# Performance work log

Measured on AMD Instinct MI355X. Metric: run time of the kernel, lower is better.

The kernel has to match this reference:

```python
import jax, jax.numpy as jnp
import numpy as np

B = 2048   # batch
C = 64     # EEG channels (num_eegch)
T = 125    # time samples -> pool5 -> 25 -> (p=5, 5)
H = 8      # num_heads
L = 6      # num_layers
D = 16     # num_projected_features
QK = 8     # qkv_len
P = 5      # tokens before cls
EPS = 1e-5


def setup_inputs() -> dict:
    key = jax.random.key(0)
    ks = iter(jax.random.split(key, 64))

    def nrm(shape, s=0.05):
        return jax.random.normal(next(ks), shape, jnp.float32) * s

    return {
        "x": jax.random.normal(next(ks), (B, 1, C, T), jnp.float32),
        "conv_t_w": nrm((8, 1, 1, 63)),
        "conv_t_b": nrm((8,)),
        "bn1_g": 1.0 + nrm((8,)),
        "bn1_b": nrm((8,)),
        "bn1_m": nrm((8,)),
        "bn1_v": 1.0 + 0.1 * jax.random.uniform(next(ks), (8,), jnp.float32),
        "conv_s_w": nrm((16, 1, C, 1)),
        "conv_s_b": nrm((16,)),
        "bn2_g": 1.0 + nrm((16,)),
        "bn2_b": nrm((16,)),
        "bn2_m": nrm((16,)),
        "bn2_v": 1.0 + 0.1 * jax.random.uniform(next(ks), (16,), jnp.float32),
        "proj_w": nrm((D, 16 * 5)),
        "proj_b": nrm((D,)),
        "cls_token": nrm((1, 1, D), 1.0),
        "pe": nrm((1, P + 1, D), 1.0),
        "qkv_w": nrm((L, 3 * H * QK, D)),
        "qkv_b": nrm((L, 3 * H * QK)),
        "out_w": nrm((L, D, H * QK)),
        "out_b": nrm((L, D)),
        "ln1_g": jnp.ones((L, D), jnp.float32),
        "ln1_b": jnp.zeros((L, D), jnp.float32),
        "ln2_g": jnp.ones((L, D), jnp.float32),
        "ln2_b": jnp.zeros((L, D), jnp.float32),
        "mlp_w1": nrm((L, 2 * D, D)),
        "mlp_b1": nrm((L, 2 * D)),
        "mlp_w2": nrm((L, D, 2 * D)),
        "mlp_b2": nrm((L, D)),
        "head_ln_g": jnp.ones((D,), jnp.float32),
        "head_ln_b": jnp.zeros((D,), jnp.float32),
        "head_w": nrm((2, D)),
        "head_b": nrm((2,)),
    }


def _bn(z, g, b, m, v):
    s = (g * jax.lax.rsqrt(v + EPS))[None, :, None, None]
    return (z - m[None, :, None, None]) * s + b[None, :, None, None]


def _ln(z, g, b):
    m = z.mean(-1, keepdims=True)
    var = jnp.mean((z - m) ** 2, -1, keepdims=True)
    return (z - m) * jax.lax.rsqrt(var + EPS) * g + b


def _forward(x, conv_t_w, conv_t_b, bn1_g, bn1_b, bn1_m, bn1_v,
             conv_s_w, conv_s_b, bn2_g, bn2_b, bn2_m, bn2_v,
             proj_w, proj_b, cls_token, pe,
             qkv_w, qkv_b, out_w, out_b, ln1_g, ln1_b, ln2_g, ln2_b,
             mlp_w1, mlp_b1, mlp_w2, mlp_b2,
             head_ln_g, head_ln_b, head_w, head_b):
    b = x.shape[0]
    dn = ('NCHW', 'OIHW', 'NCHW')
    # temporal conv, 'same' padding on width (kernel 63 -> pad 31/31)
    y = jax.lax.conv_general_dilated(x, conv_t_w, (1, 1), [(0, 0), (31, 31)], dimension_numbers=dn)
    y = _bn(y + conv_t_b[None, :, None, None], bn1_g, bn1_b, bn1_m, bn1_v)
    # grouped spatial conv collapses the EEG-channel axis
    y = jax.lax.conv_general_dilated(y, conv_s_w, (1, 1), 'VALID', dimension_numbers=dn, feature_group_count=8)
    y = _bn(y + conv_s_b[None, :, None, None], bn2_g, bn2_b, bn2_m, bn2_v)
    y = jax.nn.elu(y)                              # (b,16,1,125)
    y = y.reshape(b, 16, 1, T // 5, 5).mean(-1)    # avg_pool2d (1,5) -> (b,16,1,25)
    # dropout: identity at inference
    y = y.reshape(b, 16, 1, P, 5)
    y = jnp.swapaxes(y, 3, 4)
    tok = jnp.swapaxes(y.reshape(b, 16 * 5, P), 1, 2)   # (b,5,80)
    tok = tok @ proj_w.T + proj_b                       # (b,5,16)
    z = jnp.concatenate([jnp.broadcast_to(cls_token, (b, 1, D)), tok], axis=1) + pe  # (b,6,16)
    scale = QK ** -0.5
    for i in range(L):
        h1 = _ln(z, ln1_g[i], ln1_b[i])
        qkv = h1 @ qkv_w[i].T + qkv_b[i]                # (b,6,3*H*QK)
        q, k, v = jnp.split(qkv, 3, axis=-1)
        q = q.reshape(b, P + 1, H, QK).transpose(0, 2, 1, 3)
        k = k.reshape(b, P + 1, H, QK).transpose(0, 2, 1, 3)
        v = v.reshape(b, P + 1, H, QK).transpose(0, 2, 1, 3)
        att = jax.nn.softmax(jnp.einsum('bhsd,bhtd->bhst', q, k) * scale, axis=-1)
        o = jnp.einsum('bhst,bhtd->bhsd', att, v).transpose(0, 2, 1, 3).reshape(b, P + 1, H * QK)
        z = o @ out_w[i].T + out_b[i] + z
        h2 = _ln(z, ln2_g[i], ln2_b[i])
        m = jax.nn.gelu(h2 @ mlp_w1[i].T + mlp_b1[i], approximate=False) @ mlp_w2[i].T + mlp_b2[i]
        z = m + z
    cls = _ln(z[:, 0, :], head_ln_g, head_ln_b)
    return jax.nn.softmax(cls @ head_w.T + head_b, axis=-1)


def reference(x, conv_t_w, conv_t_b, bn1_g, bn1_b, bn1_m, bn1_v,
              conv_s_w, conv_s_b, bn2_g, bn2_b, bn2_m, bn2_v,
              proj_w, proj_b, cls_token, pe,
              qkv_w, qkv_b, out_w, out_b, ln1_g, ln1_b, ln2_g, ln2_b,
              mlp_w1, mlp_b1, mlp_w2, mlp_b2,
              head_ln_g, head_ln_b, head_w, head_b):
    return _forward(x, conv_t_w, conv_t_b, bn1_g, bn1_b, bn1_m, bn1_v,
                    conv_s_w, conv_s_b, bn2_g, bn2_b, bn2_m, bn2_v,
                    proj_w, proj_b, cls_token, pe,
                    qkv_w, qkv_b, out_w, out_b, ln1_g, ln1_b, ln2_g, ln2_b,
                    mlp_w1, mlp_b1, mlp_w2, mlp_b2,
                    head_ln_g, head_ln_b, head_w, head_b)
```

## Files before the change

### kernel.cpp

```cpp
#include <hip/hip_runtime.h>

#define WAVE_SYNC() do { asm volatile("" ::: "memory"); \
                         __builtin_amdgcn_wave_barrier(); \
                         asm volatile("" ::: "memory"); } while (0)

typedef _Float16 h2 __attribute__((ext_vector_type(2)));
typedef _Float16 h4 __attribute__((ext_vector_type(4)));
typedef _Float16 h8 __attribute__((ext_vector_type(8)));

__device__ __forceinline__ float fdot2(h2 a, h2 b, float c) {
#if defined(__has_builtin)
#if __has_builtin(__builtin_amdgcn_fdot2)
    return __builtin_amdgcn_fdot2(a, b, c, false);
#else
    return (float)a[0]*(float)b[0] + (float)a[1]*(float)b[1] + c;
#endif
#else
    return (float)a[0]*(float)b[0] + (float)a[1]*(float)b[1] + c;
#endif
}

__device__ __forceinline__ float dot8h(h8 a, h8 b, float c) {
    float s = c;
    #pragma unroll
    for (int i = 0; i < 4; ++i) {
        h2 x = {a[2*i], a[2*i+1]};
        h2 y = {b[2*i], b[2*i+1]};
        s = fdot2(x, y, s);
    }
    return s;
}

__device__ __forceinline__ float dot16h(h8 a0, h8 a1, h8 b0, h8 b1, float c) {
    return dot8h(a1, b1, dot8h(a0, b0, c));
}

__device__ __forceinline__ float ln_norm16(float z, float g, float bb) {
    float s = z, q = z * z;
    #pragma unroll
    for (int off = 8; off >= 1; off >>= 1) {
        s += __shfl_xor(s, off, 16);
        q += __shfl_xor(q, off, 16);
    }
    float mean = s * 0.0625f;
    float var  = q * 0.0625f - mean * mean;
    return (z - mean) * rsqrtf(var + 1e-5f) * g + bb;
}

__device__ __forceinline__ float gelu_exact(float a) {
    float xa = fabsf(a) * 0.70710678118654752f;
    float tt = 1.f / (1.f + 0.3275911f * xa);
    float poly = tt * (0.254829592f + tt * (-0.284496736f + tt * (1.421413741f
               + tt * (-1.453152027f + tt * 1.061405429f))));
    float erfv = 1.f - poly * __expf(-xa * xa);
    erfv = a >= 0.f ? erfv : -erfv;
    return 0.5f * a * (1.f + erfv);
}

#define F5_XSTR 210
#define F5_PF   1680
#define F5_WLH  8000
#define F5_TOTF 4512

extern "C" __global__ __launch_bounds__(128, 2)
void eegnet_frontend(
    const float* __restrict__ x,
    const float* __restrict__ conv_t_w, const float* __restrict__ conv_t_b,
    const float* __restrict__ bn1_g, const float* __restrict__ bn1_b,
    const float* __restrict__ bn1_m, const float* __restrict__ bn1_v,
    const float* __restrict__ conv_s_w, const float* __restrict__ conv_s_b,
    const float* __restrict__ bn2_g, const float* __restrict__ bn2_b,
    const float* __restrict__ bn2_m, const float* __restrict__ bn2_v,
    const float* __restrict__ proj_w, const float* __restrict__ proj_b,
    float* __restrict__ tokws)
{
    __shared__ __align__(16) float sm[F5_TOTF];
    _Float16* smh = reinterpret_cast<_Float16*>(sm);
    const int b   = blockIdx.x;
    const int tid = threadIdx.x;

    {
        const float4* xb4 = reinterpret_cast<const float4*>(x + (size_t)b * 8000);
        #pragma unroll
        for (int k = 0; k < 16; ++k) {
            int g = min(tid + k * 128, 1999);
            float4 v = xb4[g];
            h4 hv = {(_Float16)v.x, (_Float16)v.y, (_Float16)v.z, (_Float16)v.w};
            *reinterpret_cast<h4*>(&smh[4 * g]) = hv;
        }
    }
    {
        #pragma unroll
        for (int k = 0; k < 4; ++k) {
            int i  = tid + k * 128;
            int c2 = i & 31, o = i >> 5;
            float2 wv = *reinterpret_cast<const float2*>(conv_s_w + o * 64 + 2 * c2);
            h2 hp = {(_Float16)wv.x, (_Float16)wv.y};
            *reinterpret_cast<h2*>(&smh[F5_WLH + (c2 * 16 + o) * 2]) = hp;
        }
    }
    __syncthreads();

    float acc[16];
    #pragma unroll
    for (int o = 0; o < 16; ++o) acc[o] = 0.f;
    if (tid < 125) {
        #pragma unroll 4
        for (int c2 = 0; c2 < 32; ++c2) {
            h2 xp = { smh[(2 * c2) * 125 + tid], smh[(2 * c2 + 1) * 125 + tid] };
            const h8* wrow = reinterpret_cast<const h8*>(&smh[F5_WLH + c2 * 32]);
            h8 w0 = wrow[0], w1 = wrow[1], w2 = wrow[2], w3 = wrow[3];
            #pragma unroll
            for (int o = 0; o < 4; ++o) {
                h2 p0 = {w0[2*o], w0[2*o+1]};
                h2 p1 = {w1[2*o], w1[2*o+1]};
                h2 p2 = {w2[2*o], w2[2*o+1]};
                h2 p3 = {w3[2*o], w3[2*o+1]};
                acc[o]      = fdot2(p0, xp, acc[o]);
                acc[4 + o]  = fdot2(p1, xp, acc[4 + o]);
                acc[8 + o]  = fdot2(p2, xp, acc[8 + o]);
                acc[12 + o] = fdot2(p3, xp, acc[12 + o]);
            }
        }
    }
    __syncthreads();

    for (int i = tid; i < 16 * 85; i += 128) {
        int row = i / 85, k = i - row * 85;
        int off = (k < 32) ? k : (k + 125);
        smh[row * F5_XSTR + off] = (_Float16)0.f;
    }
    if (tid < 125) {
        #pragma unroll
        for (int o = 0; o < 16; ++o)
            smh[o * F5_XSTR + 32 + tid] = (_Float16)acc[o];
    }
    __syncthreads();

    const int oo = tid & 15, qg = tid >> 4, gg = oo >> 1;
    float sa, cc;
    {
        float s1 = bn1_g[gg] * rsqrtf(bn1_v[gg] + 1e-5f);
        float b1 = (conv_t_b[gg] - bn1_m[gg]) * s1 + bn1_b[gg];
        float s2 = bn2_g[oo] * rsqrtf(bn2_v[oo] + 1e-5f);
        float ssum = 0.f;
        const float4* csw = reinterpret_cast<const float4*>(conv_s_w + oo * 64);
        #pragma unroll
        for (int i = 0; i < 16; ++i) {
            float4 v = csw[i];
            ssum += v.x + v.y + v.z + v.w;
        }
        sa = s1 * s2;
        cc = (b1 * ssum + conv_s_b[oo] - bn2_m[oo]) * s2 + bn2_b[oo];
    }
    float wt[63];
    #pragma unroll
    for (int k = 0; k < 63; ++k) wt[k] = conv_t_w[gg * 63 + k];

    #pragma unroll 2
    for (int jj = 0; jj < 4; ++jj) {
        int j  = qg * 4 + jj;
        int jc = min(j, 24);
        int base = oo * F5_XSTR + 5 * jc + 1;
        float acc5[5] = {0.f, 0.f, 0.f, 0.f, 0.f};
        #pragma unroll
        for (int m = 0; m < 67; ++m) {
            float xv = (float)smh[base + m];
            #pragma unroll
            for (int u = 0; u < 5; ++u)
                if (u <= m && m - u <= 62) acc5[u] += wt[m - u] * xv;
        }
        float psum = 0.f;
        #pragma unroll
        for (int u = 0; u < 5; ++u) {
            float v = acc5[u] * sa + cc;
            psum += (v > 0.f) ? v : (__expf(v) - 1.f);
        }
        if (j == jc) sm[F5_PF + oo * 28 + j] = psum * 0.2f;
    }

    __syncthreads();

    if (tid < 80) {
        int p = tid >> 4, dd = tid & 15;
        float acc3 = proj_b[dd];
        const float4* wp = reinterpret_cast<const float4*>(proj_w + dd * 80);
        #pragma unroll
        for (int i = 0; i < 20; ++i) {
            float4 w4 = wp[i];
            acc3 += w4.x * sm[F5_PF + ((4*i+0)/5) * 28 + p * 5 + ((4*i+0)%5)];
            acc3 += w4.y * sm[F5_PF + ((4*i+1)/5) * 28 + p * 5 + ((4*i+1)%5)];
            acc3 += w4.z * sm[F5_PF + ((4*i+2)/5) * 28 + p * 5 + ((4*i+2)%5)];
            acc3 += w4.w * sm[F5_PF + ((4*i+3)/5) * 28 + p * 5 + ((4*i+3)%5)];
        }
        tokws[b * 80 + p * 16 + dd] = acc3;
    }
}

#define WQKVH 0
#define WOUTH 4608
#define WM1H  5760
#define WM2H  6528
#define BQKVF 3584
#define BOUTF 3776
#define BM1F  3792
#define BM2F  3824
#define LN1GF 3840
#define LN1BF 3856
#define LN2GF 3872
#define LN2BF 3888
#define SCR0  7808
#define SSTRH 1584
#define SH1H  0
#define SQKVH 144
#define SMHSH 1344
#define T_BYTES 18784

extern "C" __global__ __launch_bounds__(128, 2)
void eegnet_transformer(
    const float* __restrict__ cls_token, const float* __restrict__ pe,
    const float* __restrict__ qkv_w, const float* __restrict__ qkv_b,
    const float* __restrict__ out_w, const float* __restrict__ out_b,
    const float* __restrict__ ln1_g, const float* __restrict__ ln1_b,
    const float* __restrict__ ln2_g, const float* __restrict__ ln2_b,
    const float* __restrict__ mlp_w1, const float* __restrict__ mlp_b1,
    const float* __restrict__ mlp_w2, const float* __restrict__ mlp_b2,
    const float* __restrict__ head_ln_g, const float* __restrict__ head_ln_b,
    const float* __restrict__ head_w, const float* __restrict__ head_b,
    const float* __restrict__ tokws, float* __restrict__ out)
{
    __shared__ __align__(16) unsigned char smb[T_BYTES];
    float*    smf = reinterpret_cast<float*>(smb);
    _Float16* smh = reinterpret_cast<_Float16*>(smb);

    const int tid = threadIdx.x;
    const int sA  = blockIdx.x;
    const int d16 = tid & 15, qg = tid >> 4;
    const int t6c = min(qg, 5);
    const int wav = tid >> 6, al = tid & 63;
    const int sb  = SCR0;

    float zA;
    {
        float peV = pe[t6c * 16 + d16];
        if (t6c == 0) zA = cls_token[d16] + peV;
        else          zA = tokws[sA * 80 + (t6c - 1) * 16 + d16] + peV;
    }

    #pragma unroll 1
    for (int li = 0; li < 6; ++li) {
        __syncthreads();

        {
            const float4* s1 = reinterpret_cast<const float4*>(qkv_w + li * 3072);
            #pragma unroll
            for (int it = 0; it < 6; ++it) {
                int i = tid + it * 128;
                float4 v = s1[i];
                int j = i >> 2, k = (i & 3) << 2;
                h4 hv = {(_Float16)v.x, (_Float16)v.y, (_Float16)v.z, (_Float16)v.w};
                *reinterpret_cast<h4*>(&smh[WQKVH + j * 24 + k]) = hv;
            }
            const float4* s2 = reinterpret_cast<const float4*>(out_w + li * 1024);
            #pragma unroll
            for (int it = 0; it < 2; ++it) {
                int i = tid + it * 128;
                float4 v = s2[i];
                int j = i >> 4, k = (i & 15) << 2;
                h4 hv = {(_Float16)v.x, (_Float16)v.y, (_Float16)v.z, (_Float16)v.w};
                *reinterpret_cast<h4*>(&smh[WOUTH + j * 72 + k]) = hv;
            }
            {
                float4 v = reinterpret_cast<const float4*>(mlp_w1 + li * 512)[tid];
                int j = tid >> 2, k = (tid & 3) << 2;
                h4 hv = {(_Float16)v.x, (_Float16)v.y, (_Float16)v.z, (_Float16)v.w};
                *reinterpret_cast<h4*>(&smh[WM1H + j * 24 + k]) = hv;
            }
            {
                float4 v = reinterpret_cast<const float4*>(mlp_w2 + li * 512)[tid];
                int j = tid >> 3, k = (tid & 7) << 2;
                h4 hv = {(_Float16)v.x, (_Float16)v.y, (_Float16)v.z, (_Float16)v.w};
                *reinterpret_cast<h4*>(&smh[WM2H + j * 40 + k]) = hv;
            }
            #pragma unroll
            for (int p = 0; p < 2; ++p) {
                int i = tid + p * 128;
                if (i < 192)       smf[BQKVF + i]       = qkv_b[li * 192 + i];
                else if (i < 208)  smf[BOUTF + i - 192] = out_b[li * 16 + i - 192];
                else if (i < 240)  smf[BM1F + i - 208]  = mlp_b1[li * 32 + i - 208];
                else               smf[BM2F + i - 240]  = mlp_b2[li * 16 + i - 240];
            }
            if (tid >= 64 && tid < 80)        smf[LN1GF + tid - 64]  = ln1_g[li * 16 + tid - 64];
            else if (tid >= 80 && tid < 96)   smf[LN1BF + tid - 80]  = ln1_b[li * 16 + tid - 80];
            else if (tid >= 96 && tid < 112)  smf[LN2GF + tid - 96]  = ln2_g[li * 16 + tid - 96];
            else if (tid >= 112 && tid < 128) smf[LN2BF + tid - 112] = ln2_b[li * 16 + tid - 112];
        }
        __syncthreads();

        {
            float g = smf[LN1GF + d16], bb = smf[LN1BF + d16];
            smh[sb + SH1H + t6c * 24 + d16] = (_Float16)ln_norm16(zA, g, bb);
        }
        WAVE_SYNC();

        h8 hA0 = *reinterpret_cast<const h8*>(&smh[sb + SH1H + t6c * 24]);
        h8 hA1 = *reinterpret_cast<const h8*>(&smh[sb + SH1H + t6c * 24 + 8]);

        #pragma unroll 2
        for (int r = 0; r < 12; ++r) {
            int j = d16 + 16 * r;
            h8 w0 = *reinterpret_cast<const h8*>(&smh[WQKVH + j * 24]);
            h8 w1 = *reinterpret_cast<const h8*>(&smh[WQKVH + j * 24 + 8]);
            float bb = smf[BQKVF + j];
            smh[sb + SQKVH + t6c * 200 + j] = (_Float16)dot16h(hA0, hA1, w0, w1, bb);
        }
        __syncthreads();

        {
            bool act = (wav == 0) ? (al < 32) : (al < 16);
            if (act) {
                int h  = al & 7;
                int qs = (wav == 0) ? (al >> 3) : 4 + (al >> 3);
                const int qoff = sb + SQKVH + qs * 200 + h * 8;
                h8 qA = *reinterpret_cast<const h8*>(&smh[qoff]);
                float scA[6];
                #pragma unroll
                for (int t = 0; t < 6; ++t) {
                    h8 kA = *reinterpret_cast<const h8*>(&smh[sb + SQKVH + t * 200 + 64 + h * 8]);
                    scA[t] = dot8h(qA, kA, 0.f) * 0.35355339059327373f;
                }
                float mxA = scA[0];
                #pragma unroll
                for (int t = 1; t < 6; ++t) mxA = fmaxf(mxA, scA[t]);
                float suA = 0.f;
                #pragma unroll
                for (int t = 0; t < 6; ++t) { scA[t] = __expf(scA[t] - mxA); suA += scA[t]; }
                float ivA = 1.f / suA;
                h2 oA[4];
                #pragma unroll
                for (int k2 = 0; k2 < 4; ++k2) oA[k2] = h2{0, 0};
                #pragma unroll
                for (int t = 0; t < 6; ++t) {
                    h8 vA = *reinterpret_cast<const h8*>(&smh[sb + SQKVH + t * 200 + 128 + h * 8]);
                    _Float16 aa = (_Float16)(scA[t] * ivA);
                    h2 av = {aa, aa};
                    #pragma unroll
                    for (int k2 = 0; k2 < 4; ++k2) {
                        h2 va = {vA[2*k2], vA[2*k2+1]};
                        oA[k2] += av * va;
                    }
                }
                h8 stA;
                #pragma unroll
                for (int k2 = 0; k2 < 4; ++k2) {
                    stA[2*k2] = oA[k2][0]; stA[2*k2+1] = oA[k2][1];
                }
                *reinterpret_cast<h8*>(&smh[qoff]) = stA;
            }
        }
        WAVE_SYNC();

        {
            float aA = smf[BOUTF + d16];
            #pragma unroll
            for (int i = 0; i < 8; ++i) {
                h8 w  = *reinterpret_cast<const h8*>(&smh[WOUTH + d16 * 72 + 8 * i]);
                h8 va = *reinterpret_cast<const h8*>(&smh[sb + SQKVH + t6c * 200 + 8 * i]);
                aA = dot8h(va, w, aA);
            }
            zA += aA;
        }

        {
            float g = smf[LN2GF + d16], bb = smf[LN2BF + d16];
            smh[sb + SH1H + t6c * 24 + d16] = (_Float16)ln_norm16(zA, g, bb);
        }
        WAVE_SYNC();
        hA0 = *reinterpret_cast<const h8*>(&smh[sb + SH1H + t6c * 24]);
        hA1 = *reinterpret_cast<const h8*>(&smh[sb + SH1H + t6c * 24 + 8]);

        #pragma unroll
        for (int r = 0; r < 2; ++r) {
            int uu = d16 + 16 * r;
            h8 w0 = *reinterpret_cast<const h8*>(&smh[WM1H + uu * 24]);
            h8 w1 = *reinterpret_cast<const h8*>(&smh[WM1H + uu * 24 + 8]);
            float bb = smf[BM1F + uu];
            float aA = dot16h(hA0, hA1, w0, w1, bb);
            smh[sb + SMHSH + t6c * 40 + uu] = (_Float16)gelu_exact(aA);
        }
        WAVE_SYNC();

        {
            float aA = smf[BM2F + d16];
            #pragma unroll
            for (int i = 0; i < 4; ++i) {
                h8 w  = *reinterpret_cast<const h8*>(&smh[WM2H + d16 * 40 + 8 * i]);
                h8 va = *reinterpret_cast<const h8*>(&smh[sb + SMHSH + t6c * 40 + 8 * i]);
                aA = dot8h(va, w, aA);
            }
            zA += aA;
        }
    }

    if (tid < 16) {
        float g = head_ln_g[d16], bb = head_ln_b[d16];
        float w0 = head_w[d16], w1 = head_w[16 + d16];
        float cvA = ln_norm16(zA, g, bb);
        float pA0 = cvA * w0, pA1 = cvA * w1;
        #pragma unroll
        for (int off = 8; off >= 1; off >>= 1) {
            pA0 += __shfl_xor(pA0, off, 16);
            pA1 += __shfl_xor(pA1, off, 16);
        }
        if (tid == 0) {
            float l0 = pA0 + head_b[0], l1 = pA1 + head_b[1];
            float mx = fmaxf(l0, l1);
            float e0 = __expf(l0 - mx), e1 = __expf(l1 - mx);
            float inv = 1.f / (e0 + e1);
            out[sA * 2 + 0] = e0 * inv;
            out[sA * 2 + 1] = e1 * inv;
        }
    }
}

extern "C" void kernel_launch(void* const* d_in, const int* in_sizes, int n_in,
                              void* d_out, int out_size, void* d_ws, size_t ws_size,
                              hipStream_t stream) {
    (void)n_in; (void)ws_size; (void)out_size;
    const float* a0  = (const float*)d_in[0];
    const float* a1  = (const float*)d_in[1];
    const float* a2  = (const float*)d_in[2];
    const float* a3  = (const float*)d_in[3];
    const float* a4  = (const float*)d_in[4];
    const float* a5  = (const float*)d_in[5];
    const float* a6  = (const float*)d_in[6];
    const float* a7  = (const float*)d_in[7];
    const float* a8  = (const float*)d_in[8];
    const float* a9  = (const float*)d_in[9];
    const float* a10 = (const float*)d_in[10];
    const float* a11 = (const float*)d_in[11];
    const float* a12 = (const float*)d_in[12];
    const float* a13 = (const float*)d_in[13];
    const float* a14 = (const float*)d_in[14];
    const float* a15 = (const float*)d_in[15];
    const float* a16 = (const float*)d_in[16];
    const float* a17 = (const float*)d_in[17];
    const float* a18 = (const float*)d_in[18];
    const float* a19 = (const float*)d_in[19];
    const float* a20 = (const float*)d_in[20];
    const float* a21 = (const float*)d_in[21];
    const float* a22 = (const float*)d_in[22];
    const float* a23 = (const float*)d_in[23];
    const float* a24 = (const float*)d_in[24];
    const float* a25 = (const float*)d_in[25];
    const float* a26 = (const float*)d_in[26];
    const float* a27 = (const float*)d_in[27];
    const float* a28 = (const float*)d_in[28];
    const float* a29 = (const float*)d_in[29];
    const float* a30 = (const float*)d_in[30];
    const float* a31 = (const float*)d_in[31];
    const float* a32 = (const float*)d_in[32];

    int Bn = in_sizes[0] / (64 * 125);
    float* tokws = (float*)d_ws;

    eegnet_frontend<<<Bn, 128, 0, stream>>>(
        a0, a1, a2, a3, a4, a5, a6, a7, a8, a9, a10, a11, a12, a13, a14, tokws);

    eegnet_transformer<<<Bn, 128, 0, stream>>>(
        a15, a16, a17, a18, a19, a20, a21, a22, a23, a24, a25, a26, a27, a28,
        a29, a30, a31, a32, tokws, (float*)d_out);
}
```

Baseline: 240.0 us.

## Fuse EEG frontend and transformer into a single kernel

Merges the convolutional frontend and the transformer encoder into one kernel per batch element. Tokens are kept in shared memory instead of going through a global workspace, and the second launch is removed. The spatial conv switches from packed fp16 dot2 on shared-memory weights to fp32 FMAs reading weights directly from global memory. The temporal conv staging buffer is stored as fp32, and the shared-memory layout is reorganised to fit both stages.

```diff
diff --git a/kernel.cpp b/kernel.cpp
--- a/kernel.cpp
+++ b/kernel.cpp
@@ -57,145 +57,11 @@
     return 0.5f * a * (1.f + erfv);
 }
 
-#define F5_XSTR 210
-#define F5_PF   1680
-#define F5_WLH  8000
-#define F5_TOTF 4512
-
-extern "C" __global__ __launch_bounds__(128, 2)
-void eegnet_frontend(
-    const float* __restrict__ x,
-    const float* __restrict__ conv_t_w, const float* __restrict__ conv_t_b,
-    const float* __restrict__ bn1_g, const float* __restrict__ bn1_b,
-    const float* __restrict__ bn1_m, const float* __restrict__ bn1_v,
-    const float* __restrict__ conv_s_w, const float* __restrict__ conv_s_b,
-    const float* __restrict__ bn2_g, const float* __restrict__ bn2_b,
-    const float* __restrict__ bn2_m, const float* __restrict__ bn2_v,
-    const float* __restrict__ proj_w, const float* __restrict__ proj_b,
-    float* __restrict__ tokws)
-{
-    __shared__ __align__(16) float sm[F5_TOTF];
-    _Float16* smh = reinterpret_cast<_Float16*>(sm);
-    const int b   = blockIdx.x;
-    const int tid = threadIdx.x;
-
-    {
-        const float4* xb4 = reinterpret_cast<const float4*>(x + (size_t)b * 8000);
-        #pragma unroll
-        for (int k = 0; k < 16; ++k) {
-            int g = min(tid + k * 128, 1999);
-            float4 v = xb4[g];
-            h4 hv = {(_Float16)v.x, (_Float16)v.y, (_Float16)v.z, (_Float16)v.w};
-            *reinterpret_cast<h4*>(&smh[4 * g]) = hv;
-        }
-    }
-    {
-        #pragma unroll
-        for (int k = 0; k < 4; ++k) {
-            int i  = tid + k * 128;
-            int c2 = i & 31, o = i >> 5;
-            float2 wv = *reinterpret_cast<const float2*>(conv_s_w + o * 64 + 2 * c2);
-            h2 hp = {(_Float16)wv.x, (_Float16)wv.y};
-            *reinterpret_cast<h2*>(&smh[F5_WLH + (c2 * 16 + o) * 2]) = hp;
-        }
-    }
-    __syncthreads();
-
-    float acc[16];
-    #pragma unroll
-    for (int o = 0; o < 16; ++o) acc[o] = 0.f;
-    if (tid < 125) {
-        #pragma unroll 4
-        for (int c2 = 0; c2 < 32; ++c2) {
-            h2 xp = { smh[(2 * c2) * 125 + tid], smh[(2 * c2 + 1) * 125 + tid] };
-            const h8* wrow = reinterpret_cast<const h8*>(&smh[F5_WLH + c2 * 32]);
-            h8 w0 = wrow[0], w1 = wrow[1], w2 = wrow[2], w3 = wrow[3];
-            #pragma unroll
-            for (int o = 0; o < 4; ++o) {
-                h2 p0 = {w0[2*o], w0[2*o+1]};
-                h2 p1 = {w1[2*o], w1[2*o+1]};
-                h2 p2 = {w2[2*o], w2[2*o+1]};
-                h2 p3 = {w3[2*o], w3[2*o+1]};
-                acc[o]      = fdot2(p0, xp, acc[o]);
-                acc[4 + o]  = fdot2(p1, xp, acc[4 + o]);
-                acc[8 + o]  = fdot2(p2, xp, acc[8 + o]);
-                acc[12 + o] = fdot2(p3, xp, acc[12 + o]);
-            }
-        }
-    }
-    __syncthreads();
-
-    for (int i = tid; i < 16 * 85; i += 128) {
-        int row = i / 85, k = i - row * 85;
-        int off = (k < 32) ? k : (k + 125);
-        smh[row * F5_XSTR + off] = (_Float16)0.f;
-    }
-    if (tid < 125) {
-        #pragma unroll
-        for (int o = 0; o < 16; ++o)
-            smh[o * F5_XSTR + 32 + tid] = (_Float16)acc[o];
-    }
-    __syncthreads();
-
-    const int oo = tid & 15, qg = tid >> 4, gg = oo >> 1;
-    float sa, cc;
-    {
-        float s1 = bn1_g[gg] * rsqrtf(bn1_v[gg] + 1e-5f);
-        float b1 = (conv_t_b[gg] - bn1_m[gg]) * s1 + bn1_b[gg];
-        float s2 = bn2_g[oo] * rsqrtf(bn2_v[oo] + 1e-5f);
-        float ssum = 0.f;
-        const float4* csw = reinterpret_cast<const float4*>(conv_s_w + oo * 64);
-        #pragma unroll
-        for (int i = 0; i < 16; ++i) {
-            float4 v = csw[i];
-            ssum += v.x + v.y + v.z + v.w;
-        }
-        sa = s1 * s2;
-        cc = (b1 * ssum + conv_s_b[oo] - bn2_m[oo]) * s2 + bn2_b[oo];
-    }
-    float wt[63];
-    #pragma unroll
-    for (int k = 0; k < 63; ++k) wt[k] = conv_t_w[gg * 63 + k];
-
-    #pragma unroll 2
-    for (int jj = 0; jj < 4; ++jj) {
-        int j  = qg * 4 + jj;
-        int jc = min(j, 24);
-        int base = oo * F5_XSTR + 5 * jc + 1;
-        float acc5[5] = {0.f, 0.f, 0.f, 0.f, 0.f};
-        #pragma unroll
-        for (int m = 0; m < 67; ++m) {
-            float xv = (float)smh[base + m];
-            #pragma unroll
-            for (int u = 0; u < 5; ++u)
-                if (u <= m && m - u <= 62) acc5[u] += wt[m - u] * xv;
-        }
-        float psum = 0.f;
-        #pragma unroll
-        for (int u = 0; u < 5; ++u) {
-            float v = acc5[u] * sa + cc;
-            psum += (v > 0.f) ? v : (__expf(v) - 1.f);
-        }
-        if (j == jc) sm[F5_PF + oo * 28 + j] = psum * 0.2f;
-    }
-
-    __syncthreads();
-
-    if (tid < 80) {
-        int p = tid >> 4, dd = tid & 15;
-        float acc3 = proj_b[dd];
-        const float4* wp = reinterpret_cast<const float4*>(proj_w + dd * 80);
-        #pragma unroll
-        for (int i = 0; i < 20; ++i) {
-            float4 w4 = wp[i];
-            acc3 += w4.x * sm[F5_PF + ((4*i+0)/5) * 28 + p * 5 + ((4*i+0)%5)];
-            acc3 += w4.y * sm[F5_PF + ((4*i+1)/5) * 28 + p * 5 + ((4*i+1)%5)];
-            acc3 += w4.z * sm[F5_PF + ((4*i+2)/5) * 28 + p * 5 + ((4*i+2)%5)];
-            acc3 += w4.w * sm[F5_PF + ((4*i+3)/5) * 28 + p * 5 + ((4*i+3)%5)];
-        }
-        tokws[b * 80 + p * 16 + dd] = acc3;
-    }
-}
+
+#define F_XSTR 204
+#define F_PL   4000
+#define TOKF   4704
+#define FUSED_TOTF 4784
 
 #define WQKVH 0
 #define WOUTH 4608
@@ -210,14 +76,20 @@
 #define LN2GF 3872
 #define LN2BF 3888
 #define SCR0  7808
-#define SSTRH 1584
 #define SH1H  0
 #define SQKVH 144
 #define SMHSH 1344
-#define T_BYTES 18784
 
 extern "C" __global__ __launch_bounds__(128, 2)
-void eegnet_transformer(
+void eegnet_fused(
+    const float* __restrict__ x,
+    const float* __restrict__ conv_t_w, const float* __restrict__ conv_t_b,
+    const float* __restrict__ bn1_g, const float* __restrict__ bn1_b,
+    const float* __restrict__ bn1_m, const float* __restrict__ bn1_v,
+    const float* __restrict__ conv_s_w, const float* __restrict__ conv_s_b,
+    const float* __restrict__ bn2_g, const float* __restrict__ bn2_b,
+    const float* __restrict__ bn2_m, const float* __restrict__ bn2_v,
+    const float* __restrict__ proj_w, const float* __restrict__ proj_b,
     const float* __restrict__ cls_token, const float* __restrict__ pe,
     const float* __restrict__ qkv_w, const float* __restrict__ qkv_b,
     const float* __restrict__ out_w, const float* __restrict__ out_b,
@@ -227,24 +99,126 @@
     const float* __restrict__ mlp_w2, const float* __restrict__ mlp_b2,
     const float* __restrict__ head_ln_g, const float* __restrict__ head_ln_b,
     const float* __restrict__ head_w, const float* __restrict__ head_b,
-    const float* __restrict__ tokws, float* __restrict__ out)
+    float* __restrict__ out)
 {
-    __shared__ __align__(16) unsigned char smb[T_BYTES];
-    float*    smf = reinterpret_cast<float*>(smb);
-    _Float16* smh = reinterpret_cast<_Float16*>(smb);
+    __shared__ __align__(16) float sm[FUSED_TOTF];
+    _Float16* smh = reinterpret_cast<_Float16*>(sm);
+    _Float16* xr  = reinterpret_cast<_Float16*>(sm);
 
     const int tid = threadIdx.x;
-    const int sA  = blockIdx.x;
+    const int b   = blockIdx.x;
+
+    {
+        const float4* xb4 = reinterpret_cast<const float4*>(x + (size_t)b * 8000);
+        #pragma unroll
+        for (int k = 0; k < 16; ++k) {
+            int g = min(tid + k * 128, 1999);
+            float4 v = xb4[g];
+            h4 hv = {(_Float16)v.x, (_Float16)v.y, (_Float16)v.z, (_Float16)v.w};
+            *reinterpret_cast<h4*>(&xr[4 * g]) = hv;
+        }
+    }
+    __syncthreads();
+
+    float acc[16];
+    #pragma unroll
+    for (int o = 0; o < 16; ++o) acc[o] = 0.f;
+    {
+        const int t = min(tid, 124);
+        #pragma unroll 8
+        for (int c = 0; c < 64; ++c) {
+            float xv = (float)xr[c * 125 + t];
+            #pragma unroll
+            for (int o = 0; o < 16; ++o)
+                acc[o] += conv_s_w[o * 64 + c] * xv;
+        }
+    }
+    __syncthreads();
+
+    for (int i = tid; i < 16 * 79; i += 128) {
+        int row = i / 79, k = i - row * 79;
+        int off = (k < 32) ? k : (k + 125);
+        sm[row * F_XSTR + off] = 0.f;
+    }
+    if (tid < 125) {
+        #pragma unroll
+        for (int o = 0; o < 16; ++o)
+            sm[o * F_XSTR + 32 + tid] = acc[o];
+    }
+    __syncthreads();
+
+    const int oo = tid & 15, qg8 = tid >> 4, gg = oo >> 1;
+    {
+        float sa, cc;
+        {
+            float s1 = bn1_g[gg] * rsqrtf(bn1_v[gg] + 1e-5f);
+            float b1 = (conv_t_b[gg] - bn1_m[gg]) * s1 + bn1_b[gg];
+            float s2 = bn2_g[oo] * rsqrtf(bn2_v[oo] + 1e-5f);
+            float ssum = 0.f;
+            const float4* csw = reinterpret_cast<const float4*>(conv_s_w + oo * 64);
+            #pragma unroll
+            for (int i = 0; i < 16; ++i) {
+                float4 v = csw[i];
+                ssum += v.x + v.y + v.z + v.w;
+            }
+            sa = s1 * s2;
+            cc = (b1 * ssum + conv_s_b[oo] - bn2_m[oo]) * s2 + bn2_b[oo];
+        }
+        float wt[63];
+        #pragma unroll
+        for (int k = 0; k < 63; ++k) wt[k] = conv_t_w[gg * 63 + k];
+
+        #pragma unroll 2
+        for (int jj = 0; jj < 4; ++jj) {
+            int j  = qg8 * 4 + jj;
+            int jc = min(j, 24);
+            int base = oo * F_XSTR + 5 * jc + 1;
+            float acc5[5] = {0.f, 0.f, 0.f, 0.f, 0.f};
+            #pragma unroll
+            for (int m = 0; m < 67; ++m) {
+                float xv = sm[base + m];
+                #pragma unroll
+                for (int u = 0; u < 5; ++u)
+                    if (u <= m && m - u <= 62) acc5[u] += wt[m - u] * xv;
+            }
+            float psum = 0.f;
+            #pragma unroll
+            for (int u = 0; u < 5; ++u) {
+                float v = acc5[u] * sa + cc;
+                psum += (v > 0.f) ? v : (__expf(v) - 1.f);
+            }
+            if (j == jc) sm[F_PL + oo * 28 + j] = psum * 0.2f;
+        }
+    }
+    __syncthreads();
+
+    if (tid < 80) {
+        int p = tid >> 4, dd = tid & 15;
+        float acc3 = proj_b[dd];
+        const float4* wp = reinterpret_cast<const float4*>(proj_w + dd * 80);
+        #pragma unroll
+        for (int i = 0; i < 20; ++i) {
+            float4 w4 = wp[i];
+            acc3 += w4.x * sm[F_PL + ((4*i+0)/5) * 28 + p * 5 + ((4*i+0)%5)];
+            acc3 += w4.y * sm[F_PL + ((4*i+1)/5) * 28 + p * 5 + ((4*i+1)%5)];
+            acc3 += w4.z * sm[F_PL + ((4*i+2)/5) * 28 + p * 5 + ((4*i+2)%5)];
+            acc3 += w4.w * sm[F_PL + ((4*i+3)/5) * 28 + p * 5 + ((4*i+3)%5)];
+        }
+        sm[TOKF + p * 16 + dd] = acc3;
+    }
+    __syncthreads();
+
     const int d16 = tid & 15, qg = tid >> 4;
     const int t6c = min(qg, 5);
     const int wav = tid >> 6, al = tid & 63;
     const int sb  = SCR0;
+    const int sA  = blockIdx.x;
 
     float zA;
     {
         float peV = pe[t6c * 16 + d16];
         if (t6c == 0) zA = cls_token[d16] + peV;
-        else          zA = tokws[sA * 80 + (t6c - 1) * 16 + d16] + peV;
+        else          zA = sm[TOKF + (t6c - 1) * 16 + d16] + peV;
     }
 
     #pragma unroll 1
@@ -285,20 +259,20 @@
             #pragma unroll
             for (int p = 0; p < 2; ++p) {
                 int i = tid + p * 128;
-                if (i < 192)       smf[BQKVF + i]       = qkv_b[li * 192 + i];
-                else if (i < 208)  smf[BOUTF + i - 192] = out_b[li * 16 + i - 192];
-                else if (i < 240)  smf[BM1F + i - 208]  = mlp_b1[li * 32 + i - 208];
-                else               smf[BM2F + i - 240]  = mlp_b2[li * 16 + i - 240];
-            }
-            if (tid >= 64 && tid < 80)        smf[LN1GF + tid - 64]  = ln1_g[li * 16 + tid - 64];
-            else if (tid >= 80 && tid < 96)   smf[LN1BF + tid - 80]  = ln1_b[li * 16 + tid - 80];
-            else if (tid >= 96 && tid < 112)  smf[LN2GF + tid - 96]  = ln2_g[li * 16 + tid - 96];
-            else if (tid >= 112 && tid < 128) smf[LN2BF + tid - 112] = ln2_b[li * 16 + tid - 112];
+                if (i < 192)       sm[BQKVF + i]       = qkv_b[li * 192 + i];
+                else if (i < 208)  sm[BOUTF + i - 192] = out_b[li * 16 + i - 192];
+                else if (i < 240)  sm[BM1F + i - 208]  = mlp_b1[li * 32 + i - 208];
+                else               sm[BM2F + i - 240]  = mlp_b2[li * 16 + i - 240];
+            }
+            if (tid >= 64 && tid < 80)        sm[LN1GF + tid - 64]  = ln1_g[li * 16 + tid - 64];
+            else if (tid >= 80 && tid < 96)   sm[LN1BF + tid - 80]  = ln1_b[li * 16 + tid - 80];
+            else if (tid >= 96 && tid < 112)  sm[LN2GF + tid - 96]  = ln2_g[li * 16 + tid - 96];
+            else if (tid >= 112 && tid < 128) sm[LN2BF + tid - 112] = ln2_b[li * 16 + tid - 112];
         }
         __syncthreads();
 
         {
-            float g = smf[LN1GF + d16], bb = smf[LN1BF + d16];
+            float g = sm[LN1GF + d16], bb = sm[LN1BF + d16];
             smh[sb + SH1H + t6c * 24 + d16] = (_Float16)ln_norm16(zA, g, bb);
         }
         WAVE_SYNC();
@@ -311,7 +285,7 @@
             int j = d16 + 16 * r;
             h8 w0 = *reinterpret_cast<const h8*>(&smh[WQKVH + j * 24]);
             h8 w1 = *reinterpret_cast<const h8*>(&smh[WQKVH + j * 24 + 8]);
-            float bb = smf[BQKVF + j];
+            float bb = sm[BQKVF + j];
             smh[sb + SQKVH + t6c * 200 + j] = (_Float16)dot16h(hA0, hA1, w0, w1, bb);
         }
         __syncthreads();
@@ -361,18 +335,18 @@
         WAVE_SYNC();
 
         {
-            float aA = smf[BOUTF + d16];
+            float aA = sm[BOUTF + d16];
             #pragma unroll
             for (int i = 0; i < 8; ++i) {
-                h8 w  = *reinterpret_cast<const h8*>(&smh[WOUTH + d16 * 72 + 8 * i]);
+                h8 wv = *reinterpret_cast<const h8*>(&smh[WOUTH + d16 * 72 + 8 * i]);
                 h8 va = *reinterpret_cast<const h8*>(&smh[sb + SQKVH + t6c * 200 + 8 * i]);
-                aA = dot8h(va, w, aA);
+                aA = dot8h(va, wv, aA);
             }
             zA += aA;
         }
 
         {
-            float g = smf[LN2GF + d16], bb = smf[LN2BF + d16];
+            float g = sm[LN2GF + d16], bb = sm[LN2BF + d16];
             smh[sb + SH1H + t6c * 24 + d16] = (_Float16)ln_norm16(zA, g, bb);
         }
         WAVE_SYNC();
@@ -384,19 +358,19 @@
             int uu = d16 + 16 * r;
             h8 w0 = *reinterpret_cast<const h8*>(&smh[WM1H + uu * 24]);
             h8 w1 = *reinterpret_cast<const h8*>(&smh[WM1H + uu * 24 + 8]);
-            float bb = smf[BM1F + uu];
+            float bb = sm[BM1F + uu];
             float aA = dot16h(hA0, hA1, w0, w1, bb);
             smh[sb + SMHSH + t6c * 40 + uu] = (_Float16)gelu_exact(aA);
         }
         WAVE_SYNC();
 
         {
-            float aA = smf[BM2F + d16];
+            float aA = sm[BM2F + d16];
             #pragma unroll
             for (int i = 0; i < 4; ++i) {
-                h8 w  = *reinterpret_cast<const h8*>(&smh[WM2H + d16 * 40 + 8 * i]);
+                h8 wv = *reinterpret_cast<const h8*>(&smh[WM2H + d16 * 40 + 8 * i]);
                 h8 va = *reinterpret_cast<const h8*>(&smh[sb + SMHSH + t6c * 40 + 8 * i]);
-                aA = dot8h(va, w, aA);
+                aA = dot8h(va, wv, aA);
             }
             zA += aA;
         }
@@ -426,7 +400,7 @@
 extern "C" void kernel_launch(void* const* d_in, const int* in_sizes, int n_in,
                               void* d_out, int out_size, void* d_ws, size_t ws_size,
                               hipStream_t stream) {
-    (void)n_in; (void)ws_size; (void)out_size;
+    (void)n_in; (void)ws_size; (void)out_size; (void)d_ws;
     const float* a0  = (const float*)d_in[0];
     const float* a1  = (const float*)d_in[1];
     const float* a2  = (const float*)d_in[2];
@@ -462,12 +436,9 @@
     const float* a32 = (const float*)d_in[32];
 
     int Bn = in_sizes[0] / (64 * 125);
-    float* tokws = (float*)d_ws;
-
-    eegnet_frontend<<<Bn, 128, 0, stream>>>(
-        a0, a1, a2, a3, a4, a5, a6, a7, a8, a9, a10, a11, a12, a13, a14, tokws);
-
-    eegnet_transformer<<<Bn, 128, 0, stream>>>(
-        a15, a16, a17, a18, a19, a20, a21, a22, a23, a24, a25, a26, a27, a28,
-        a29, a30, a31, a32, tokws, (float*)d_out);
-}
+
+    eegnet_fused<<<Bn, 128, 0, stream>>>(
+        a0, a1, a2, a3, a4, a5, a6, a7, a8, a9, a10, a11, a12,
+        a13, a14, a15, a16, a17, a18, a19, a20, a21, a22, a23, a24,
+        a25, a26, a27, a28, a29, a30, a31, a32, (float*)d_out);
+}
```

After: 252.5 us. +5.2%, slower.
